# Kernel tuning notes

Measured on AMD Instinct MI355X. Metric: run time of the kernel, lower is better.

Reference implementation:

```python
import jax, jax.numpy as jnp
import numpy as np

HEADS = 16


def setup_inputs() -> dict:
    key = jax.random.key(0)
    ks = jax.random.split(key, 7)
    b, n, dim = 4, 1024, 1024
    s = 1.0 / np.sqrt(dim)
    return {
        "x": jax.random.normal(ks[0], (b, n, dim), dtype=jnp.float32),
        "Wq": jax.random.normal(ks[1], (dim, dim), dtype=jnp.float32) * s,
        "bq": jax.random.normal(ks[2], (dim,), dtype=jnp.float32) * 0.01,
        "Wv": jax.random.normal(ks[3], (dim, dim), dtype=jnp.float32) * s,
        "bv": jax.random.normal(ks[4], (dim,), dtype=jnp.float32) * 0.01,
        "Wo": jax.random.normal(ks[5], (dim, dim), dtype=jnp.float32) * s,
        "bo": jax.random.normal(ks[6], (dim,), dtype=jnp.float32) * 0.01,
    }


def reference(x, Wq, bq, Wv, bv, Wo, bo):
    b, n, dim = x.shape
    h = HEADS
    d = dim // h
    scale = d ** -0.5

    # projections (torch Linear: x @ W.T + b), split heads: b n (h d) -> b h n d
    q = (x @ Wq.T + bq).reshape(b, n, h, d).transpose(0, 2, 1, 3)
    v = (x @ Wv.T + bv).reshape(b, n, h, d).transpose(0, 2, 1, 3)

    # pairwise L2 distance scores: ||q_i||^2 - 2 q_i.q_j + ||q_j||^2
    dots = jnp.einsum("bhnd,bhmd->bhnm", q, q)          # [b,h,n,n]
    sq = jnp.sum(q * q, axis=-1)                          # [b,h,n]
    scores = -(sq[..., :, None] - 2.0 * dots + sq[..., None, :]) * scale
    attn = jax.nn.softmax(scores, axis=-1)

    out = jnp.einsum("bhnm,bhmd->bhnd", attn, v)          # [b,h,n,d]
    out = out.transpose(0, 2, 1, 3).reshape(b, n, dim)    # b h n d -> b n (h d)
    return out @ Wo.T + bo
```

## Files before the change

kernel.cpp:

```cpp
#include <hip/hip_runtime.h>
#include <hip/hip_bf16.h>

typedef __hip_bfloat16 bf16;
typedef short short8 __attribute__((ext_vector_type(8)));
typedef float floatx4 __attribute__((ext_vector_type(4)));
typedef unsigned uintx4 __attribute__((ext_vector_type(4)));
typedef unsigned short ushort;

#define MFMA __builtin_amdgcn_mfma_f32_16x16x32_bf16

#define BATCH 4
#define SEQ   1024
#define DIM   1024
#define HEADS 16
#define HD    64
#define RS    72


__device__ __forceinline__ float b2f(ushort u) {
    union { unsigned i; float f; } x; x.i = (unsigned)u << 16; return x.f;
}
__device__ __forceinline__ ushort f2b(float f) {
    union { float f; unsigned i; } x; x.f = f;
    return (ushort)((x.i + 0x7FFFu + ((x.i >> 16) & 1u)) >> 16);
}

__device__ __forceinline__ void nts16(void* p, uint4 v) {
    uintx4 x; x.x = v.x; x.y = v.y; x.z = v.z; x.w = v.w;
    __builtin_nontemporal_store(x, (uintx4*)p);
}
__device__ __forceinline__ void nts16f(void* p, float4 v) {
    floatx4 x; x.x = v.x; x.y = v.y; x.z = v.z; x.w = v.w;
    __builtin_nontemporal_store(x, (floatx4*)p);
}
__device__ __forceinline__ void nts2(ushort* p, ushort v) {
    __builtin_nontemporal_store(v, p);
}

__device__ __forceinline__ void gload16(const ushort* gp, ushort* lp) {
    __builtin_amdgcn_global_load_lds(
        (const __attribute__((address_space(1))) unsigned*)gp,
        (__attribute__((address_space(3))) unsigned*)lp, 16, 0, 0);
}

__device__ __forceinline__ short8 cvt8(uint4 a, uint4 b) {
    const float* f0 = (const float*)&a;
    const float* f1 = (const float*)&b;
    union { __hip_bfloat162 h; unsigned u; } c0, c1, c2, c3;
    float2 p;
    p.x = f0[0]; p.y = f0[1]; c0.h = __float22bfloat162_rn(p);
    p.x = f0[2]; p.y = f0[3]; c1.h = __float22bfloat162_rn(p);
    p.x = f1[0]; p.y = f1[1]; c2.h = __float22bfloat162_rn(p);
    p.x = f1[2]; p.y = f1[3]; c3.h = __float22bfloat162_rn(p);
    short8 s;
    unsigned* su = (unsigned*)&s;
    su[0] = c0.u; su[1] = c1.u; su[2] = c2.u; su[3] = c3.u;
    return s;
}

__global__ __launch_bounds__(256)
void conv_x(const float* __restrict__ x, ushort* __restrict__ xb)
{
    const size_t g = (size_t)blockIdx.x * 256 + threadIdx.x;
    const uint4* xv = (const uint4*)x;
    uint4 a = xv[g * 2], b = xv[g * 2 + 1];
    short8 s = cvt8(a, b);
    nts16(xb + g * 8, *(uint4*)&s);
}

template<int OUT>
__global__ __launch_bounds__(256, 3)
void gemm_core(const ushort* __restrict__ Ab,
               const float* __restrict__ W0, const float* __restrict__ b0,
               const float* __restrict__ W1, const float* __restrict__ b1,
               ushort* __restrict__ Qd, ushort* __restrict__ Vd,
               float* __restrict__ Fd, float* __restrict__ sqQ)
{
    __shared__ __align__(16) ushort SMEM[2 * 8192 + 2 * 64 * RS];
    const int t = threadIdx.x;
    const int w = t >> 6, lane = t & 63;
    const int lr = lane & 15, quad = lane >> 4;
    const int isV = (!OUT) && (blockIdx.x >= 16);
    const int n0 = (blockIdx.x & 15) * 64;
    const int m0 = blockIdx.y * 128;
    const float* __restrict__ W    = isV ? W1 : W0;
    const float* __restrict__ bias = isV ? b1 : b0;
    const int mw = (w >> 1) * 64, nw = (w & 1) * 32;
    const int ar = t >> 3, ac8 = (t & 7) * 8;
    const int arow = lane >> 3;
    const int acS  = ((lane & 7) ^ arow) * 8;

    ushort* Acur = SMEM;
    ushort* Anxt = SMEM + 8192;
    ushort* Bcur = SMEM + 16384;
    ushort* Bnxt = SMEM + 16384 + 64 * RS;

    uint4 wpre[4];
    #pragma unroll
    for (int c = 0; c < 2; ++c) {
        const float* wp = W + (size_t)(n0 + c * 32 + ar) * DIM + ac8;
        wpre[2 * c]     = *(const uint4*)wp;
        wpre[2 * c + 1] = *(const uint4*)(wp + 4);
    }
    #pragma unroll
    for (int i = 0; i < 4; ++i) {
        const int chunk = w * 4 + i;
        gload16(Ab + (size_t)(m0 + chunk * 8 + arow) * DIM + acS,
                Acur + chunk * 512);
    }
    #pragma unroll
    for (int c = 0; c < 2; ++c)
        *(short8*)&Bcur[(c * 32 + ar) * RS + ac8] = cvt8(wpre[2 * c], wpre[2 * c + 1]);
    __syncthreads();

    floatx4 acc[4][2];
    const floatx4 fz = {0.f, 0.f, 0.f, 0.f};
    #pragma unroll
    for (int i = 0; i < 4; ++i)
        #pragma unroll
        for (int j = 0; j < 2; ++j) acc[i][j] = fz;

    for (int kt = 0; kt < 16; ++kt) {
        if (kt < 15) {
            const int k0 = (kt + 1) * 64;
            #pragma unroll
            for (int i = 0; i < 4; ++i) {
                const int chunk = w * 4 + i;
                gload16(Ab + (size_t)(m0 + chunk * 8 + arow) * DIM + k0 + acS,
                        Anxt + chunk * 512);
            }
            #pragma unroll
            for (int c = 0; c < 2; ++c) {
                const float* wp = W + (size_t)(n0 + c * 32 + ar) * DIM + k0 + ac8;
                wpre[2 * c]     = *(const uint4*)wp;
                wpre[2 * c + 1] = *(const uint4*)(wp + 4);
            }
        }
        #pragma unroll
        for (int ks = 0; ks < 2; ++ks) {
            short8 af[4], bfx[2];
            #pragma unroll
            for (int tm = 0; tm < 4; ++tm) {
                const int rowa = mw + tm * 16 + lr;
                const int csw  = (((ks << 2) | quad) ^ (lr & 7)) * 8;
                af[tm] = *(const short8*)&Acur[rowa * 64 + csw];
            }
            #pragma unroll
            for (int tn = 0; tn < 2; ++tn)
                bfx[tn] = *(const short8*)&Bcur[(nw + tn * 16 + lr) * RS + ks * 32 + quad * 8];
            #pragma unroll
            for (int tm = 0; tm < 4; ++tm)
                #pragma unroll
                for (int tn = 0; tn < 2; ++tn)
                    acc[tm][tn] = MFMA(af[tm], bfx[tn], acc[tm][tn], 0, 0, 0);
        }
        if (kt < 15) {
            #pragma unroll
            for (int c = 0; c < 2; ++c)
                *(short8*)&Bnxt[(c * 32 + ar) * RS + ac8] = cvt8(wpre[2 * c], wpre[2 * c + 1]);
        }
        __syncthreads();
        ushort* tp;
        tp = Acur; Acur = Anxt; Anxt = tp;
        tp = Bcur; Bcur = Bnxt; Bnxt = tp;
    }

    if (OUT) {
        float* TF = (float*)SMEM;
        #pragma unroll
        for (int pass = 0; pass < 2; ++pass) {
            __syncthreads();
            if ((w >> 1) == pass) {
                #pragma unroll
                for (int tn = 0; tn < 2; ++tn) {
                    const float bval = bias[n0 + nw + tn * 16 + lr];
                    #pragma unroll
                    for (int tm = 0; tm < 4; ++tm)
                        #pragma unroll
                        for (int r = 0; r < 4; ++r)
                            TF[(tm * 16 + quad * 4 + r) * 68 + nw + tn * 16 + lr] =
                                acc[tm][tn][r] + bval;
                }
            }
            __syncthreads();
            #pragma unroll
            for (int it = 0; it < 4; ++it) {
                const int cid = it * 256 + t;
                const int row = cid >> 4, c4 = (cid & 15) * 4;
                nts16f(Fd + (size_t)(m0 + pass * 64 + row) * DIM + n0 + c4,
                       *(const float4*)&TF[row * 68 + c4]);
            }
        }
        return;
    }

    const int bb = m0 >> 10, ii0 = m0 & 1023;
    const int head = blockIdx.x & 15;
    const int bh = bb * HEADS + head;
    if (!isV) {
        #pragma unroll
        for (int tn = 0; tn < 2; ++tn) {
            const float bval = bias[n0 + nw + tn * 16 + lr];
            #pragma unroll
            for (int tm = 0; tm < 4; ++tm)
                #pragma unroll
                for (int r = 0; r < 4; ++r)
                    SMEM[(mw + tm * 16 + quad * 4 + r) * 80 + nw + tn * 16 + lr] =
                        f2b(acc[tm][tn][r] + bval);
        }
        __syncthreads();
        {
            const int row = t >> 1, half = t & 1;
            float s = 0.f;
            #pragma unroll
            for (int c = 0; c < 4; ++c) {
                uint4 kk = *(const uint4*)&SMEM[row * 80 + half * 32 + c * 8];
                const ushort* u = (const ushort*)&kk;
                #pragma unroll
                for (int e = 0; e < 8; ++e) { float f = b2f(u[e]); s += f * f; }
            }
            s += __shfl_xor(s, 1);
            if (half == 0) sqQ[(size_t)bh * SEQ + ii0 + row] = s;
        }
        #pragma unroll
        for (int it = 0; it < 4; ++it) {
            const int cid = it * 256 + t;
            const int row = cid >> 3, col8 = (cid & 7) * 8;
            nts16(Qd + ((size_t)bh * SEQ + ii0 + row) * HD + col8,
                  *(const uint4*)&SMEM[row * 80 + col8]);
        }
    } else {
        #pragma unroll
        for (int tn = 0; tn < 2; ++tn) {
            const float bval = bias[n0 + nw + tn * 16 + lr];
            #pragma unroll
            for (int tm = 0; tm < 4; ++tm)
                #pragma unroll
                for (int r = 0; r < 4; ++r)
                    SMEM[(nw + tn * 16 + lr) * 144 + mw + tm * 16 + quad * 4 + r] =
                        f2b(acc[tm][tn][r] + bval);
        }
        __syncthreads();
        #pragma unroll
        for (int it = 0; it < 4; ++it) {
            const int cid = it * 256 + t;
            const int row = cid >> 4, col8 = (cid & 15) * 8;
            nts16(Vd + ((size_t)bh * HD + row) * SEQ + ii0 + col8,
                  *(const uint4*)&SMEM[row * 144 + col8]);
        }
    }
}

__global__ __launch_bounds__(256, 3)
void attn_mfma(const ushort* __restrict__ Q, const ushort* __restrict__ Vt,
               const float* __restrict__ sqG, ushort* __restrict__ O)
{
    __shared__ __align__(16) ushort Ps[128 * RS];
    __shared__ __align__(16) ushort KV[4 * 4096];

    const int t = threadIdx.x;
    const int w = t >> 6, lane = t & 63;
    const int lr = lane & 15, quad = lane >> 4;
    const int id = blockIdx.x;
    const int bh = id & 63;
    const int i0 = (id >> 6) * 128;
    const ushort* __restrict__ Qp = Q  + (size_t)bh * SEQ * HD;
    const ushort* __restrict__ Vp = Vt + (size_t)bh * HD * SEQ;
    const float*  __restrict__ sqB = sqG + (size_t)bh * SEQ;

    const int arow = lane >> 3;
    const int acS  = ((lane & 7) ^ arow) * 8;

    ushort* Kcur = KV;
    ushort* Vcur = KV + 4096;
    ushort* Knxt = KV + 8192;
    ushort* Vnxt = KV + 12288;

    #pragma unroll
    for (int i = 0; i < 2; ++i) {
        const int c = w + i * 4;
        gload16(Qp + (size_t)(c * 8 + arow) * HD + acS, Kcur + c * 512);
        gload16(Vp + (size_t)(c * 8 + arow) * SEQ + acS, Vcur + c * 512);
    }
    #pragma unroll
    for (int it = 0; it < 4; ++it) {
        const int cid = it * 256 + t;
        const int r = cid >> 3, c8 = (cid & 7) * 8;
        *(uint4*)&Ps[r * RS + c8] = *(const uint4*)(Qp + (size_t)(i0 + r) * HD + c8);
    }
    __syncthreads();

    short8 qa[2][2];
    #pragma unroll
    for (int tm = 0; tm < 2; ++tm)
        #pragma unroll
        for (int ks = 0; ks < 2; ++ks)
            qa[tm][ks] = *(const short8*)&Ps[(w * 32 + tm * 16 + lr) * RS + ks * 32 + quad * 8];
    float sqi[2][4];
    #pragma unroll
    for (int tm = 0; tm < 2; ++tm)
        #pragma unroll
        for (int r = 0; r < 4; ++r)
            sqi[tm][r] = sqB[i0 + w * 32 + tm * 16 + quad * 4 + r];

    floatx4 oacc[2][4];
    const floatx4 fz = {0.f, 0.f, 0.f, 0.f};
    float lrow[2][4] = {};
    #pragma unroll
    for (int tm = 0; tm < 2; ++tm)
        #pragma unroll
        for (int td = 0; td < 4; ++td) oacc[tm][td] = fz;

    for (int jt = 0; jt < 16; ++jt) {
        if (jt < 15) {
            const int j0n = (jt + 1) * 64;
            #pragma unroll
            for (int i = 0; i < 2; ++i) {
                const int c = w + i * 4;
                gload16(Qp + (size_t)(j0n + c * 8 + arow) * HD + acS, Knxt + c * 512);
                gload16(Vp + (size_t)(c * 8 + arow) * SEQ + j0n + acS, Vnxt + c * 512);
            }
        }
        float sq4[4];
        #pragma unroll
        for (int tn = 0; tn < 4; ++tn) sq4[tn] = sqB[jt * 64 + tn * 16 + lr];

        short8 kb[4][2];
        #pragma unroll
        for (int tn = 0; tn < 4; ++tn)
            #pragma unroll
            for (int ks = 0; ks < 2; ++ks) {
                const int row = tn * 16 + lr;
                kb[tn][ks] = *(const short8*)&Kcur[row * 64 + ((((ks << 2) | quad)) ^ (lr & 7)) * 8];
            }

        #pragma unroll
        for (int tm = 0; tm < 2; ++tm) {
            floatx4 sacc[4];
            #pragma unroll
            for (int tn = 0; tn < 4; ++tn) {
                floatx4 a = MFMA(qa[tm][0], kb[tn][0], fz, 0, 0, 0);
                sacc[tn]  = MFMA(qa[tm][1], kb[tn][1], a, 0, 0, 0);
            }
            float sc[4][4];
            #pragma unroll
            for (int tn = 0; tn < 4; ++tn) {
                const float msq = -0.125f * sq4[tn];
                #pragma unroll
                for (int r = 0; r < 4; ++r)
                    sc[tn][r] = __expf(0.25f * sacc[tn][r] + msq - 0.125f * sqi[tm][r]);
            }
            #pragma unroll
            for (int r = 0; r < 4; ++r)
                lrow[tm][r] += sc[0][r] + sc[1][r] + sc[2][r] + sc[3][r];
            #pragma unroll
            for (int tp = 0; tp < 2; ++tp)
                #pragma unroll
                for (int r = 0; r < 4; ++r) {
                    float2 fp; fp.x = sc[2 * tp][r]; fp.y = sc[2 * tp + 1][r];
                    union { __hip_bfloat162 h; unsigned u; } cv;
                    cv.h = __float22bfloat162_rn(fp);
                    const int rowb = (w * 32 + tm * 16 + quad * 4 + r) * RS + lr;
                    Ps[rowb + (2 * tp) * 16]     = (ushort)(cv.u & 0xffffu);
                    Ps[rowb + (2 * tp + 1) * 16] = (ushort)(cv.u >> 16);
                }
        }
        short8 pa[2][2], vb[4][2];
        #pragma unroll
        for (int tm = 0; tm < 2; ++tm)
            #pragma unroll
            for (int ks = 0; ks < 2; ++ks)
                pa[tm][ks] = *(const short8*)&Ps[(w * 32 + tm * 16 + lr) * RS + ks * 32 + quad * 8];
        #pragma unroll
        for (int td = 0; td < 4; ++td)
            #pragma unroll
            for (int ks = 0; ks < 2; ++ks) {
                const int row = td * 16 + lr;
                vb[td][ks] = *(const short8*)&Vcur[row * 64 + ((((ks << 2) | quad)) ^ (lr & 7)) * 8];
            }
        #pragma unroll
        for (int tm = 0; tm < 2; ++tm)
            #pragma unroll
            for (int td = 0; td < 4; ++td) {
                oacc[tm][td] = MFMA(pa[tm][0], vb[td][0], oacc[tm][td], 0, 0, 0);
                oacc[tm][td] = MFMA(pa[tm][1], vb[td][1], oacc[tm][td], 0, 0, 0);
            }
        __syncthreads();
        ushort* tp2;
        tp2 = Kcur; Kcur = Knxt; Knxt = tp2;
        tp2 = Vcur; Vcur = Vnxt; Vnxt = tp2;
    }

    const int bb = bh >> 4, head = bh & 15;
    #pragma unroll
    for (int tm = 0; tm < 2; ++tm)
        #pragma unroll
        for (int r = 0; r < 4; ++r) {
            float l = lrow[tm][r];
            l += __shfl_xor(l, 1);
            l += __shfl_xor(l, 2);
            l += __shfl_xor(l, 4);
            l += __shfl_xor(l, 8);
            const float inv = 1.f / l;
            const int row = i0 + w * 32 + tm * 16 + quad * 4 + r;
            #pragma unroll
            for (int td = 0; td < 4; ++td) {
                nts2(O + (size_t)(bb * SEQ + row) * DIM + head * HD + td * 16 + lr,
                     f2b(oacc[tm][td][r] * inv));
            }
        }
}

extern "C" void kernel_launch(void* const* d_in, const int* in_sizes, int n_in,
                              void* d_out, int out_size, void* d_ws, size_t ws_size,
                              hipStream_t stream)
{
    const float* x  = (const float*)d_in[0];
    const float* Wq = (const float*)d_in[1];
    const float* bq = (const float*)d_in[2];
    const float* Wv = (const float*)d_in[3];
    const float* bv = (const float*)d_in[4];
    const float* Wo = (const float*)d_in[5];
    const float* bo = (const float*)d_in[6];

    ushort* Qh = (ushort*)d_ws;
    ushort* Vt = Qh + (size_t)BATCH * HEADS * SEQ * HD;
    ushort* R  = Vt + (size_t)BATCH * HEADS * SEQ * HD;
    const size_t WS3 = (size_t)3 * BATCH * HEADS * SEQ * HD * 2;
    const size_t SQB = (size_t)BATCH * HEADS * SEQ * 4;
    float* sqG = (ws_size >= WS3 + SQB) ? (float*)((char*)d_ws + WS3)
                                        : (float*)d_out;

    conv_x<<<2048, 256, 0, stream>>>(x, R);
    gemm_core<0><<<dim3(32, 32), 256, 0, stream>>>(R, Wq, bq, Wv, bv, Qh, Vt,
                                                   nullptr, sqG);
    attn_mfma<<<512, 256, 0, stream>>>(Qh, Vt, sqG, R);
    gemm_core<1><<<dim3(16, 32), 256, 0, stream>>>(R, Wo, bo, nullptr, nullptr,
                                                   nullptr, nullptr,
                                                   (float*)d_out, nullptr);
}
```

Before: 186.5 us.

## Pre-convert weights to bf16 once and DMA them straight into LDS

```diff
diff --git a/kernel.cpp b/kernel.cpp
--- a/kernel.cpp
+++ b/kernel.cpp
@@ -59,20 +59,31 @@
 }
 
 __global__ __launch_bounds__(256)
-void conv_x(const float* __restrict__ x, ushort* __restrict__ xb)
+void conv_all(const float* __restrict__ x,  const float* __restrict__ Wq,
+              const float* __restrict__ Wv, const float* __restrict__ Wo,
+              ushort* __restrict__ xb,  ushort* __restrict__ wqb,
+              ushort* __restrict__ wvb, ushort* __restrict__ wob, int doWo)
 {
-    const size_t g = (size_t)blockIdx.x * 256 + threadIdx.x;
-    const uint4* xv = (const uint4*)x;
-    uint4 a = xv[g * 2], b = xv[g * 2 + 1];
-    short8 s = cvt8(a, b);
-    nts16(xb + g * 8, *(uint4*)&s);
-}
-
-template<int OUT>
+    const int b = blockIdx.x;
+    const float* src; ushort* dst; size_t off;
+    if (b < 2048)      { src = x;  dst = xb;  off = (size_t)b * 256; }
+    else if (b < 2560) { src = Wq; dst = wqb; off = (size_t)(b - 2048) * 256; }
+    else if (b < 3072) { src = Wv; dst = wvb; off = (size_t)(b - 2560) * 256; }
+    else               { if (!doWo) return;
+                         src = Wo; dst = wob; off = (size_t)(b - 3072) * 256; }
+    off += threadIdx.x;
+    const uint4* sv = (const uint4*)src;
+    uint4 a = sv[off * 2], c = sv[off * 2 + 1];
+    short8 s = cvt8(a, c);
+    nts16(dst + off * 8, *(uint4*)&s);
+}
+
+template<int OUT, int BDMA>
 __global__ __launch_bounds__(256, 3)
 void gemm_core(const ushort* __restrict__ Ab,
-               const float* __restrict__ W0, const float* __restrict__ b0,
-               const float* __restrict__ W1, const float* __restrict__ b1,
+               const ushort* __restrict__ Wb0, const ushort* __restrict__ Wb1,
+               const float* __restrict__ Wf,
+               const float* __restrict__ b0, const float* __restrict__ b1,
                ushort* __restrict__ Qd, ushort* __restrict__ Vd,
                float* __restrict__ Fd, float* __restrict__ sqQ)
 {
@@ -83,8 +94,8 @@
     const int isV = (!OUT) && (blockIdx.x >= 16);
     const int n0 = (blockIdx.x & 15) * 64;
     const int m0 = blockIdx.y * 128;
-    const float* __restrict__ W    = isV ? W1 : W0;
-    const float* __restrict__ bias = isV ? b1 : b0;
+    const ushort* __restrict__ Wb   = isV ? Wb1 : Wb0;
+    const float*  __restrict__ bias = isV ? b1 : b0;
     const int mw = (w >> 1) * 64, nw = (w & 1) * 32;
     const int ar = t >> 3, ac8 = (t & 7) * 8;
     const int arow = lane >> 3;
@@ -93,24 +104,33 @@
     ushort* Acur = SMEM;
     ushort* Anxt = SMEM + 8192;
     ushort* Bcur = SMEM + 16384;
-    ushort* Bnxt = SMEM + 16384 + 64 * RS;
+    ushort* Bnxt = SMEM + 16384 + (BDMA ? 4096 : 64 * RS);
 
     uint4 wpre[4];
-    #pragma unroll
-    for (int c = 0; c < 2; ++c) {
-        const float* wp = W + (size_t)(n0 + c * 32 + ar) * DIM + ac8;
-        wpre[2 * c]     = *(const uint4*)wp;
-        wpre[2 * c + 1] = *(const uint4*)(wp + 4);
-    }
     #pragma unroll
     for (int i = 0; i < 4; ++i) {
         const int chunk = w * 4 + i;
         gload16(Ab + (size_t)(m0 + chunk * 8 + arow) * DIM + acS,
                 Acur + chunk * 512);
     }
-    #pragma unroll
-    for (int c = 0; c < 2; ++c)
-        *(short8*)&Bcur[(c * 32 + ar) * RS + ac8] = cvt8(wpre[2 * c], wpre[2 * c + 1]);
+    if (BDMA) {
+        #pragma unroll
+        for (int i = 0; i < 2; ++i) {
+            const int c = w * 2 + i;
+            gload16(Wb + (size_t)(n0 + c * 8 + arow) * DIM + acS,
+                    Bcur + c * 512);
+        }
+    } else {
+        #pragma unroll
+        for (int c = 0; c < 2; ++c) {
+            const float* wp = Wf + (size_t)(n0 + c * 32 + ar) * DIM + ac8;
+            wpre[2 * c]     = *(const uint4*)wp;
+            wpre[2 * c + 1] = *(const uint4*)(wp + 4);
+        }
+        #pragma unroll
+        for (int c = 0; c < 2; ++c)
+            *(short8*)&Bcur[(c * 32 + ar) * RS + ac8] = cvt8(wpre[2 * c], wpre[2 * c + 1]);
+    }
     __syncthreads();
 
     floatx4 acc[4][2];
@@ -129,11 +149,20 @@
                 gload16(Ab + (size_t)(m0 + chunk * 8 + arow) * DIM + k0 + acS,
                         Anxt + chunk * 512);
             }
-            #pragma unroll
-            for (int c = 0; c < 2; ++c) {
-                const float* wp = W + (size_t)(n0 + c * 32 + ar) * DIM + k0 + ac8;
-                wpre[2 * c]     = *(const uint4*)wp;
-                wpre[2 * c + 1] = *(const uint4*)(wp + 4);
+            if (BDMA) {
+                #pragma unroll
+                for (int i = 0; i < 2; ++i) {
+                    const int c = w * 2 + i;
+                    gload16(Wb + (size_t)(n0 + c * 8 + arow) * DIM + k0 + acS,
+                            Bnxt + c * 512);
+                }
+            } else {
+                #pragma unroll
+                for (int c = 0; c < 2; ++c) {
+                    const float* wp = Wf + (size_t)(n0 + c * 32 + ar) * DIM + k0 + ac8;
+                    wpre[2 * c]     = *(const uint4*)wp;
+                    wpre[2 * c + 1] = *(const uint4*)(wp + 4);
+                }
             }
         }
         #pragma unroll
@@ -146,15 +175,22 @@
                 af[tm] = *(const short8*)&Acur[rowa * 64 + csw];
             }
             #pragma unroll
-            for (int tn = 0; tn < 2; ++tn)
-                bfx[tn] = *(const short8*)&Bcur[(nw + tn * 16 + lr) * RS + ks * 32 + quad * 8];
+            for (int tn = 0; tn < 2; ++tn) {
+                const int rowb = nw + tn * 16 + lr;
+                if (BDMA) {
+                    const int csw = (((ks << 2) | quad) ^ (lr & 7)) * 8;
+                    bfx[tn] = *(const short8*)&Bcur[rowb * 64 + csw];
+                } else {
+                    bfx[tn] = *(const short8*)&Bcur[rowb * RS + ks * 32 + quad * 8];
+                }
+            }
             #pragma unroll
             for (int tm = 0; tm < 4; ++tm)
                 #pragma unroll
                 for (int tn = 0; tn < 2; ++tn)
                     acc[tm][tn] = MFMA(af[tm], bfx[tn], acc[tm][tn], 0, 0, 0);
         }
-        if (kt < 15) {
+        if (!BDMA && kt < 15) {
             #pragma unroll
             for (int c = 0; c < 2; ++c)
                 *(short8*)&Bnxt[(c * 32 + ar) * RS + ac8] = cvt8(wpre[2 * c], wpre[2 * c + 1]);
@@ -427,15 +463,25 @@
     ushort* Vt = Qh + (size_t)BATCH * HEADS * SEQ * HD;
     ushort* R  = Vt + (size_t)BATCH * HEADS * SEQ * HD;
     const size_t WS3 = (size_t)3 * BATCH * HEADS * SEQ * HD * 2;
-    const size_t SQB = (size_t)BATCH * HEADS * SEQ * 4;
-    float* sqG = (ws_size >= WS3 + SQB) ? (float*)((char*)d_ws + WS3)
-                                        : (float*)d_out;
-
-    conv_x<<<2048, 256, 0, stream>>>(x, R);
-    gemm_core<0><<<dim3(32, 32), 256, 0, stream>>>(R, Wq, bq, Wv, bv, Qh, Vt,
-                                                   nullptr, sqG);
+    const size_t WOB = (size_t)DIM * DIM * 2;
+    const int doWo = ws_size >= WS3 + WOB;
+    ushort* Wob = (ushort*)((char*)d_ws + WS3);
+
+    ushort* Wqb = (ushort*)d_out;
+    ushort* Wvb = Wqb + (size_t)DIM * DIM;
+    float*  sqG = (float*)(Wvb + (size_t)DIM * DIM);
+
+    conv_all<<<3584, 256, 0, stream>>>(x, Wq, Wv, Wo, R, Wqb, Wvb, Wob, doWo);
+    gemm_core<0, 1><<<dim3(32, 32), 256, 0, stream>>>(R, Wqb, Wvb, nullptr,
+                                                      bq, bv, Qh, Vt, nullptr, sqG);
     attn_mfma<<<512, 256, 0, stream>>>(Qh, Vt, sqG, R);
-    gemm_core<1><<<dim3(16, 32), 256, 0, stream>>>(R, Wo, bo, nullptr, nullptr,
-                                                   nullptr, nullptr,
-                                                   (float*)d_out, nullptr);
-}
+    if (doWo) {
+        gemm_core<1, 1><<<dim3(16, 32), 256, 0, stream>>>(R, Wob, nullptr, nullptr,
+                                                          bo, nullptr, nullptr, nullptr,
+                                                          (float*)d_out, nullptr);
+    } else {
+        gemm_core<1, 0><<<dim3(16, 32), 256, 0, stream>>>(R, nullptr, nullptr, Wo,
+                                                          bo, nullptr, nullptr, nullptr,
+                                                          (float*)d_out, nullptr);
+    }
+}
```

Measured after the change: 171.7 us. -7.9%, faster.
